# Optimization experiments

Measured on AMD Instinct MI355X. Metric: run time of the kernel, lower is better.

Reference implementation:

```python
import jax, jax.numpy as jnp
import numpy as np

N, E, R, D, S = 50000, 400000, 500, 128, 20
P = R * S
EPS = 1e-5

def setup_inputs() -> dict:
    key = jax.random.key(0)
    ks = jax.random.split(key, 20)
    xav = (2.0 / (D + D)) ** 0.5  # xavier_normal std for square layers
    def W(k):
        return jax.random.normal(k, (D, D), jnp.float32) * xav
    inp = {
        'ent_emb': jax.random.normal(ks[0], (N, D), jnp.float32),
        'rel_emb': jax.random.normal(ks[1], (R, D), jnp.float32),
        'edge_Wo': W(ks[2]), 'edge_bo': jnp.zeros((D,), jnp.float32),
        'edge_Wi': W(ks[3]), 'edge_bi': jnp.zeros((D,), jnp.float32),
        'edge_g': jnp.ones((D,), jnp.float32), 'edge_b': jnp.zeros((D,), jnp.float32),
        'node_Wo': W(ks[4]), 'node_bo': jnp.zeros((D,), jnp.float32),
        'node_Wi': W(ks[5]), 'node_bi': jnp.zeros((D,), jnp.float32),
        'node_g': jnp.ones((D,), jnp.float32), 'node_b': jnp.zeros((D,), jnp.float32),
        'comp_Wo': W(ks[6]), 'comp_bo': jnp.zeros((D,), jnp.float32),
        'comp_Wi': W(ks[7]), 'comp_bi': jnp.zeros((D,), jnp.float32),
        'comp_g': jnp.ones((D,), jnp.float32), 'comp_b': jnp.zeros((D,), jnp.float32),
        'relW': W(ks[8]), 'relb': jnp.zeros((D,), jnp.float32),
        'src': jax.random.randint(ks[9], (E,), 0, N),
        'dst': jax.random.randint(ks[10], (E,), 0, N),
        'etype': jax.random.randint(ks[11], (E,), 0, R),
        'heads': jax.random.randint(ks[13], (P,), 0, N),
        'tails': jax.random.randint(ks[14], (P,), 0, N),
        'rel_ids': jnp.repeat(jnp.arange(R), S),  # S sampled pairs per relation
    }
    in_mask = jax.random.randint(ks[12], (E,), 0, 2).astype(bool)
    inp['in_mask'] = in_mask
    inp['out_mask'] = ~in_mask  # DGL forward/reverse edge split: complementary masks
    return inp

def _edge_softmax(logit, dst, n):
    # segment softmax over edges grouped by destination node
    m = jax.ops.segment_max(logit, dst, num_segments=n)
    e = jnp.exp(logit - m[dst])
    s = jax.ops.segment_sum(e, dst, num_segments=n)
    return e / s[dst]

def _in_out(x, in_m, out_m, Wo, bo, Wi, bi):
    ho = x @ Wo.T + bo
    hi = x @ Wi.T + bi
    h = jnp.where(out_m[:, None], ho, jnp.zeros((), x.dtype))
    return jnp.where(in_m[:, None], hi, h)  # in-edges overwrite (masks disjoint)

def _bn_tanh(x, g, b):
    # training-mode BatchNorm1d (biased batch variance) + Tanh
    mu = jnp.mean(x, 0)
    var = jnp.mean(jnp.square(x - mu), 0)
    return jnp.tanh(g * (x - mu) * jax.lax.rsqrt(var + EPS) + b)

def reference(ent_emb, rel_emb,
              edge_Wo, edge_bo, edge_Wi, edge_bi, edge_g, edge_b,
              node_Wo, node_bo, node_Wi, node_bi, node_g, node_b,
              comp_Wo, comp_bo, comp_Wi, comp_bi, comp_g, comp_b,
              relW, relb,
              src, dst, etype, in_mask, out_mask, heads, tails, rel_ids):
    n = ent_emb.shape[0]
    r = rel_emb.shape[0]
    rel_e = rel_emb[etype]      # [E,D]
    e_src = ent_emb[src]        # [E,D]
    e_dst = ent_emb[dst]        # [E,D]

    # EdgeLayer: attn = e_dot_v(rel_e, dst_emb)
    a = _edge_softmax(jnp.sum(rel_e * e_dst, -1), dst, n)
    h = _in_out(rel_e, in_mask, out_mask, edge_Wo, edge_bo, edge_Wi, edge_bi) * a[:, None]
    edge_ent = _bn_tanh(jax.ops.segment_sum(h, dst, num_segments=n), edge_g, edge_b)

    # NodeLayer: attn = u_dot_v, message = src emb
    a = _edge_softmax(jnp.sum(e_src * e_dst, -1), dst, n)
    h = _in_out(e_src, in_mask, out_mask, node_Wo, node_bo, node_Wi, node_bi) * a[:, None]
    node_ent = _bn_tanh(jax.ops.segment_sum(h, dst, num_segments=n), node_g, node_b)

    # CompLayer (comp_fn='mul'): comp = u_mul_e, attn = e_dot_v(comp, dst)
    comp = e_src * rel_e
    a = _edge_softmax(jnp.sum(comp * e_dst, -1), dst, n)
    h = _in_out(comp, in_mask, out_mask, comp_Wo, comp_bo, comp_Wi, comp_bi) * a[:, None]
    comp_ent = _bn_tanh(jax.ops.segment_sum(h, dst, num_segments=n), comp_g, comp_b)

    final_ent = comp_ent + ent_emb + edge_ent + node_ent

    # update_relations: mean of w_rel_edge(tail - head) per relation
    pair = ent_emb[tails] - ent_emb[heads]          # [P,D]
    upd = pair @ relW.T + relb
    ssum = jax.ops.segment_sum(upd, rel_ids, num_segments=r)
    cnt = jax.ops.segment_sum(jnp.ones((rel_ids.shape[0],), jnp.float32), rel_ids, num_segments=r)
    cnt = jnp.maximum(cnt, 1.0)[:, None]
    final_rel = rel_emb + jnp.tanh(ssum / cnt)
    return final_ent, final_rel
```

## Files before the change

kernel.cpp:

```cpp
#include <hip/hip_runtime.h>
#include <stdint.h>

#define DN 128
#define NSTAT 64

typedef short s16x8 __attribute__((ext_vector_type(8)));
typedef float f32x4 __attribute__((ext_vector_type(4)));

__device__ __forceinline__ float bfs(unsigned short u){ return __uint_as_float(((uint32_t)u) << 16); }
__device__ __forceinline__ uint32_t f2bf(float f){
    uint32_t x = __float_as_uint(f);
    return (x + 0x7FFFu + ((x >> 16) & 1u)) >> 16;
}
__device__ __forceinline__ uint32_t packbf(float a, float b){ return f2bf(a) | (f2bf(b) << 16); }
__device__ __forceinline__ float tanh_(float x){
    float e = __expf(2.0f * x);
    return 1.0f - 2.0f / (e + 1.0f);
}

struct WC { const float* src[6]; };
__global__ void k_pre(const int* dst, int* counts,
                      const uint32_t* maskw, int nwords, int* flag,
                      WC wc, unsigned short* wcv, int E){
    int gid = blockIdx.x * 256 + threadIdx.x;
    if (gid < E) atomicAdd(&counts[dst[gid]], 1);
    if (gid < nwords && maskw[gid] > 1u) atomicOr(flag, 1);
    if (gid < 6 * 16384){
        int m = gid >> 14, o = gid & 16383;
        wcv[(size_t)m * 16384 + o] = (unsigned short)f2bf(wc.src[m][o]);
    }
}

__global__ void k_scan_a(const int* counts, int* bsums){
    int t = threadIdx.x;
    int s = counts[blockIdx.x * 256 + t];
    #pragma unroll
    for (int o = 32; o; o >>= 1) s += __shfl_xor(s, o);
    __shared__ int wsum[4];
    if ((t & 63) == 0) wsum[t >> 6] = s;
    __syncthreads();
    if (t == 0) bsums[blockIdx.x] = wsum[0] + wsum[1] + wsum[2] + wsum[3];
}

__global__ void k_scan_bc(const int* counts, const int* bsums, int nsb,
                          int* rowst, int* cursor, int npad, int E){
    __shared__ int pref;
    __shared__ int wsum[4];
    __shared__ int buf[256];
    int t = threadIdx.x, bid = blockIdx.x;
    int s = (t < bid && t < nsb) ? bsums[t] : 0;
    #pragma unroll
    for (int o = 32; o; o >>= 1) s += __shfl_xor(s, o);
    if ((t & 63) == 0) wsum[t >> 6] = s;
    __syncthreads();
    if (t == 0) pref = wsum[0] + wsum[1] + wsum[2] + wsum[3];
    int i = bid * 256 + t;
    int c = counts[i];
    buf[t] = c;
    __syncthreads();
    for (int o = 1; o < 256; o <<= 1){
        int add = (t >= o) ? buf[t - o] : 0;
        __syncthreads();
        buf[t] += add;
        __syncthreads();
    }
    int rsv = buf[t] - c + pref;
    rowst[i] = rsv; cursor[i] = rsv;
    if (i == npad - 1) rowst[npad] = E;
}

__global__ void k_scatter(const int* dst, const int* src, const int* etype,
                          const unsigned char* mask8, const int* flagp,
                          int* cursor, uint32_t* epack, int E){
    int e = blockIdx.x * blockDim.x + threadIdx.x;
    if (e >= E) return;
    int bmode = *flagp;
    int mk = bmode ? (int)mask8[e] : ((const int*)mask8)[e];
    int pos = atomicAdd(&cursor[dst[e]], 1);
    epack[pos] = ((uint32_t)src[e] << 16) | ((uint32_t)etype[e] << 1) | (uint32_t)(mk != 0);
}

__global__ __launch_bounds__(256)
void k_node(const float4* ent4, const float4* rel4,
            const uint32_t* epack, const int* rowst,
            uint32_t* Sw, float* Rv, int Nn, int npad)
{
    int t = threadIdx.x, lane = t & 63, wv = t >> 6;
    int v = blockIdx.x * 4 + wv;
    if (v >= npad) return;
    int sl = lane & 31, half = lane >> 5;

    float4 d4 = {0.f, 0.f, 0.f, 0.f};
    int deg = 0, rs = 0;
    if (v < Nn){
        rs = rowst[v]; deg = rowst[v + 1] - rs;
        d4 = ent4[(size_t)v * 32 + sl];
    }
    float m0 = -1e30f, m1 = -1e30f, m2 = -1e30f;
    float si0 = 0, si1 = 0, si2 = 0, so0 = 0, so1 = 0, so2 = 0;
    float4 aI0 = {0,0,0,0}, aO0 = {0,0,0,0};
    float4 aI1 = {0,0,0,0}, aO1 = {0,0,0,0};
    float4 aI2 = {0,0,0,0}, aO2 = {0,0,0,0};

    for (int base = 0; base < deg; base += 64){
        int nb = min(64, deg - base);
        uint32_t pk = 0;
        if (lane < nb) pk = epack[rs + base + lane];
        int npair = (nb + 1) >> 1;
        for (int j = 0; j < npair; ++j){
            int ei = 2 * j + half;
            uint32_t w = (uint32_t)__shfl((int)pk, ei);
            int sj = (int)(w >> 16);
            int tj = (int)((w >> 1) & 0x7FFF);
            float mk = (float)(w & 1u);
            bool pad = (ei >= nb);
            float4 s4 = ent4[(size_t)sj * 32 + sl];
            float4 r4 = rel4[(size_t)tj * 32 + sl];
            float4 c4 = { s4.x*r4.x, s4.y*r4.y, s4.z*r4.z, s4.w*r4.w };
            float p0 = r4.x*d4.x + r4.y*d4.y + r4.z*d4.z + r4.w*d4.w;
            float p1 = s4.x*d4.x + s4.y*d4.y + s4.z*d4.z + s4.w*d4.w;
            float p2 = c4.x*d4.x + c4.y*d4.y + c4.z*d4.z + c4.w*d4.w;
            #pragma unroll
            for (int o = 1; o < 32; o <<= 1){
                p0 += __shfl_xor(p0, o);
                p1 += __shfl_xor(p1, o);
                p2 += __shfl_xor(p2, o);
            }
            if (pad){ p0 = -1e38f; p1 = -1e38f; p2 = -1e38f; }
            {
                float nm = fmaxf(m0, p0);
                float f = __expf(m0 - nm);
                si0 *= f; so0 *= f;
                aI0.x*=f; aI0.y*=f; aI0.z*=f; aI0.w*=f;
                aO0.x*=f; aO0.y*=f; aO0.z*=f; aO0.w*=f;
                m0 = nm;
                float e = __expf(p0 - m0);
                float ein = e * mk, eout = e - ein;
                si0 += ein; so0 += eout;
                aI0.x += ein*r4.x; aI0.y += ein*r4.y; aI0.z += ein*r4.z; aI0.w += ein*r4.w;
                aO0.x += eout*r4.x; aO0.y += eout*r4.y; aO0.z += eout*r4.z; aO0.w += eout*r4.w;
            }
            {
                float nm = fmaxf(m1, p1);
                float f = __expf(m1 - nm);
                si1 *= f; so1 *= f;
                aI1.x*=f; aI1.y*=f; aI1.z*=f; aI1.w*=f;
                aO1.x*=f; aO1.y*=f; aO1.z*=f; aO1.w*=f;
                m1 = nm;
                float e = __expf(p1 - m1);
                float ein = e * mk, eout = e - ein;
                si1 += ein; so1 += eout;
                aI1.x += ein*s4.x; aI1.y += ein*s4.y; aI1.z += ein*s4.z; aI1.w += ein*s4.w;
                aO1.x += eout*s4.x; aO1.y += eout*s4.y; aO1.z += eout*s4.z; aO1.w += eout*s4.w;
            }
            {
                float nm = fmaxf(m2, p2);
                float f = __expf(m2 - nm);
                si2 *= f; so2 *= f;
                aI2.x*=f; aI2.y*=f; aI2.z*=f; aI2.w*=f;
                aO2.x*=f; aO2.y*=f; aO2.z*=f; aO2.w*=f;
                m2 = nm;
                float e = __expf(p2 - m2);
                float ein = e * mk, eout = e - ein;
                si2 += ein; so2 += eout;
                aI2.x += ein*c4.x; aI2.y += ein*c4.y; aI2.z += ein*c4.z; aI2.w += ein*c4.w;
                aO2.x += eout*c4.x; aO2.y += eout*c4.y; aO2.z += eout*c4.z; aO2.w += eout*c4.w;
            }
        }
    }

    {
        float mo, nm, f;
#define MRG(m, si, so, aI, aO)                                            \
        mo = __shfl_xor(m, 32);                                           \
        nm = fmaxf(m, mo);                                                \
        f = __expf(m - nm);                                               \
        si *= f; so *= f;                                                 \
        aI.x*=f; aI.y*=f; aI.z*=f; aI.w*=f;                               \
        aO.x*=f; aO.y*=f; aO.z*=f; aO.w*=f;                               \
        si += __shfl_xor(si, 32);                                         \
        so += __shfl_xor(so, 32);                                         \
        aI.x += __shfl_xor(aI.x, 32); aI.y += __shfl_xor(aI.y, 32);       \
        aI.z += __shfl_xor(aI.z, 32); aI.w += __shfl_xor(aI.w, 32);       \
        aO.x += __shfl_xor(aO.x, 32); aO.y += __shfl_xor(aO.y, 32);       \
        aO.z += __shfl_xor(aO.z, 32); aO.w += __shfl_xor(aO.w, 32);
        MRG(m0, si0, so0, aI0, aO0)
        MRG(m1, si1, so1, aI1, aO1)
        MRG(m2, si2, so2, aI2, aO2)
#undef MRG
    }

    if (half == 0){
        uint2* S2 = (uint2*)Sw;
        size_t s2 = (size_t)npad * 32;
        size_t wi = (size_t)v * 32 + sl;
        float st, inv;
        st = si0 + so0; inv = st > 0.f ? 1.f / st : 0.f;
        S2[0*s2 + wi] = make_uint2(packbf(aI0.x*inv, aI0.y*inv), packbf(aI0.z*inv, aI0.w*inv));
        S2[1*s2 + wi] = make_uint2(packbf(aO0.x*inv, aO0.y*inv), packbf(aO0.z*inv, aO0.w*inv));
        float ri0 = si0*inv, ro0 = so0*inv;
        st = si1 + so1; inv = st > 0.f ? 1.f / st : 0.f;
        S2[2*s2 + wi] = make_uint2(packbf(aI1.x*inv, aI1.y*inv), packbf(aI1.z*inv, aI1.w*inv));
        S2[3*s2 + wi] = make_uint2(packbf(aO1.x*inv, aO1.y*inv), packbf(aO1.z*inv, aO1.w*inv));
        float ri1 = si1*inv, ro1 = so1*inv;
        st = si2 + so2; inv = st > 0.f ? 1.f / st : 0.f;
        S2[4*s2 + wi] = make_uint2(packbf(aI2.x*inv, aI2.y*inv), packbf(aI2.z*inv, aI2.w*inv));
        S2[5*s2 + wi] = make_uint2(packbf(aO2.x*inv, aO2.y*inv), packbf(aO2.z*inv, aO2.w*inv));
        float ri2 = si2*inv, ro2 = so2*inv;
        if (sl == 0){
            Rv[0*(size_t)npad + v] = ri0; Rv[1*(size_t)npad + v] = ro0;
            Rv[2*(size_t)npad + v] = ri1; Rv[3*(size_t)npad + v] = ro1;
            Rv[4*(size_t)npad + v] = ri2; Rv[5*(size_t)npad + v] = ro2;
        }
    }
}

struct GArgs {
    const short* Wi[3]; const short* Wo[3];
    const float* bi[3]; const float* bo[3];
};

__global__ __launch_bounds__(256)
void k_gemm(GArgs ga, const short* Sb, const float* Rv, unsigned short* P,
            float* statsP, int npad, int Nn)
{
    __shared__ float lsum[128], lsq[128];
    int t = threadIdx.x;
    if (t < 128){ lsum[t] = 0.f; lsq[t] = 0.f; }
    __syncthreads();
    int l = blockIdx.y;
    int lane = t & 63, wv = t >> 6;
    int lo = lane & 15, hi = lane >> 4;
    int r0 = blockIdx.x * 64 + wv * 16;
    size_t sstride = (size_t)npad * DN;
    const short* Sin  = Sb + (size_t)(2*l)   * sstride;
    const short* Sout = Sb + (size_t)(2*l+1) * sstride;
    const short* Wi = ga.Wi[l]; const short* Wo = ga.Wo[l];

    s16x8 ain[4], aout[4];
    #pragma unroll
    for (int kb = 0; kb < 4; ++kb){
        size_t o = (size_t)(r0 + lo) * DN + kb*32 + hi*8;
        ain[kb]  = *(const s16x8*)(Sin + o);
        aout[kb] = *(const s16x8*)(Sout + o);
    }
    float rin[4], rout[4];
    const float* RvI = Rv + (size_t)(2*l)   * npad;
    const float* RvO = Rv + (size_t)(2*l+1) * npad;
    #pragma unroll
    for (int rg = 0; rg < 4; ++rg){
        int vr = r0 + hi*4 + rg;
        rin[rg] = RvI[vr]; rout[rg] = RvO[vr];
    }
    unsigned short* Pl = P + (size_t)l * sstride;

    #pragma unroll
    for (int ct = 0; ct < 8; ++ct){
        f32x4 acc = {0.f, 0.f, 0.f, 0.f};
        #pragma unroll
        for (int kb = 0; kb < 4; ++kb){
            size_t wo = (size_t)(ct*16 + lo) * DN + kb*32 + hi*8;
            s16x8 bwi = *(const s16x8*)(Wi + wo);
            acc = __builtin_amdgcn_mfma_f32_16x16x32_bf16(ain[kb], bwi, acc, 0, 0, 0);
            s16x8 bwo = *(const s16x8*)(Wo + wo);
            acc = __builtin_amdgcn_mfma_f32_16x16x32_bf16(aout[kb], bwo, acc, 0, 0, 0);
        }
        int j = ct*16 + lo;
        float biv = ga.bi[l][j], bov = ga.bo[l][j];
        float cs = 0.f, cq = 0.f;
        #pragma unroll
        for (int rg = 0; rg < 4; ++rg){
            float pv = acc[rg] + rin[rg]*biv + rout[rg]*bov;
            Pl[(size_t)(r0 + hi*4 + rg) * DN + j] = (unsigned short)f2bf(pv);
            cs += pv; cq += pv*pv;
        }
        cs += __shfl_xor(cs, 16); cs += __shfl_xor(cs, 32);
        cq += __shfl_xor(cq, 16); cq += __shfl_xor(cq, 32);
        if (lane < 16){ atomicAdd(&lsum[j], cs); atomicAdd(&lsq[j], cq); }
    }
    __syncthreads();
    float* stats = statsP + (size_t)((blockIdx.x ^ (blockIdx.y << 4)) & (NSTAT-1)) * 768;
    if (t < 128){
        atomicAdd(&stats[l*128 + t], lsum[t]);
        atomicAdd(&stats[384 + l*128 + t], lsq[t]);
    }
}

struct BArgs { const float* g[3]; const float* b[3]; };

__global__ void k_bn(BArgs ba, const float* statsP, float* bnAB, int Nn){
    int t = threadIdx.x;
    if (t >= 384) return;
    float su = 0.f, sq = 0.f;
    for (int k = 0; k < NSTAT; ++k){
        su += statsP[(size_t)k * 768 + t];
        sq += statsP[(size_t)k * 768 + 384 + t];
    }
    int l = t >> 7;
    float mu = su / (float)Nn;
    float var = fmaxf(sq / (float)Nn - mu*mu, 0.f);
    float inv = rsqrtf(var + 1e-5f);
    float g = ba.g[l][t & 127], b = ba.b[l][t & 127];
    bnAB[t] = g * inv;
    bnAB[384 + t] = b - mu * g * inv;
}

__global__ __launch_bounds__(256)
void k_fin(const unsigned short* Pb, const float* bnAB,
           const float* ent, const float* relW, const float* relb,
           const float* rel, const int* heads, const int* tails,
           float* outp, int Nn, int npad, int FB, int Sp)
{
    int t = threadIdx.x, bid = blockIdx.x;
    if (bid < FB){
        __shared__ float sAB[768];
        for (int i = t; i < 768; i += 256) sAB[i] = bnAB[i];
        __syncthreads();
        int gid = bid * 256 + t;
        if (gid >= Nn * 32) return;
        int v = gid >> 5, q4 = (gid & 31) * 4;
        size_t pst = (size_t)npad * DN;
        size_t pb = (size_t)v * DN + q4;
        ushort4 p0 = *(const ushort4*)(Pb + pb);
        ushort4 p1 = *(const ushort4*)(Pb + pst + pb);
        ushort4 p2 = *(const ushort4*)(Pb + 2*pst + pb);
        float4 e4 = *(const float4*)(ent + (size_t)v * DN + q4);
        float pe[4] = { e4.x, e4.y, e4.z, e4.w };
        unsigned short pu[3][4] = { {p0.x, p0.y, p0.z, p0.w},
                                    {p1.x, p1.y, p1.z, p1.w},
                                    {p2.x, p2.y, p2.z, p2.w} };
        float o[4];
        #pragma unroll
        for (int q = 0; q < 4; ++q){
            float s = pe[q];
            #pragma unroll
            for (int l = 0; l < 3; ++l){
                int jj = l*128 + q4 + q;
                s += tanh_(sAB[jj] * bfs(pu[l][q]) + sAB[384 + jj]);
            }
            o[q] = s;
        }
        float4 ov = { o[0], o[1], o[2], o[3] };
        *(float4*)(outp + (size_t)v * DN + q4) = ov;
    } else {
        __shared__ float mp[256];
        int rr = (bid - FB) * 2 + (t >> 7);
        int j = t & 127;
        float acc = 0.f;
        for (int s = 0; s < Sp; ++s){
            int p = rr * Sp + s;
            acc += ent[(size_t)tails[p] * DN + j] - ent[(size_t)heads[p] * DN + j];
        }
        mp[t] = acc / (float)Sp;
        __syncthreads();
        float dot = relb[j];
        const float4* wr = (const float4*)(relW + (size_t)j * DN);
        const float* mpr = mp + (t >> 7) * 128;
        #pragma unroll 8
        for (int kb = 0; kb < 32; ++kb){
            float4 w = wr[kb];
            dot += mpr[kb*4+0]*w.x + mpr[kb*4+1]*w.y + mpr[kb*4+2]*w.z + mpr[kb*4+3]*w.w;
        }
        outp[(size_t)Nn * DN + (size_t)rr * DN + j] = rel[(size_t)rr * DN + j] + tanh_(dot);
    }
}

extern "C" void kernel_launch(void* const* d_in, const int* in_sizes, int n_in,
                              void* d_out, int out_size, void* d_ws, size_t ws_size,
                              hipStream_t stream)
{
    const float* entf = (const float*)d_in[0];
    const float* relf = (const float*)d_in[1];
    const float* eWo = (const float*)d_in[2];  const float* ebo = (const float*)d_in[3];
    const float* eWi = (const float*)d_in[4];  const float* ebi = (const float*)d_in[5];
    const float* eg  = (const float*)d_in[6];  const float* eb  = (const float*)d_in[7];
    const float* nWo = (const float*)d_in[8];  const float* nbo = (const float*)d_in[9];
    const float* nWi = (const float*)d_in[10]; const float* nbi = (const float*)d_in[11];
    const float* ng  = (const float*)d_in[12]; const float* nb_ = (const float*)d_in[13];
    const float* cWo = (const float*)d_in[14]; const float* cbo = (const float*)d_in[15];
    const float* cWi = (const float*)d_in[16]; const float* cbi = (const float*)d_in[17];
    const float* cg  = (const float*)d_in[18]; const float* cb  = (const float*)d_in[19];
    const float* relWs  = (const float*)d_in[20];
    const float* relb32 = (const float*)d_in[21];
    const int* srcp   = (const int*)d_in[22];
    const int* dstp   = (const int*)d_in[23];
    const int* etyp   = (const int*)d_in[24];
    const int* headsp = (const int*)d_in[25];
    const int* tailsp = (const int*)d_in[26];
    const unsigned char* mask8 = (const unsigned char*)d_in[28];

    int Nn = in_sizes[0] / DN;
    int Rr = in_sizes[1] / DN;
    int E  = in_sizes[22];
    int Pp = in_sizes[25];
    int Sp = Pp / Rr;
    int npad = ((Nn + 255) / 256) * 256;
    int nsb = npad / 256;

    char* w = (char*)d_ws; size_t off = 0;
    auto carve = [&](size_t b) -> void* {
        void* p = w + off; off = (off + b + 255) & ~(size_t)255; return p;
    };
    int*   flag   = (int*)  carve(4);
    int*   counts = (int*)  carve((size_t)npad * 4);
    float* statsP = (float*)carve((size_t)NSTAT * 768 * 4);
    size_t zlen = off;
    int*   rowst  = (int*)  carve((size_t)(npad + 1) * 4);
    int*   cursor = (int*)  carve((size_t)npad * 4);
    uint32_t* epack = (uint32_t*)carve((size_t)E * 4);
    int*   bsums  = (int*)  carve(1024 * 4);
    unsigned short* wcv = (unsigned short*)carve((size_t)6 * 16384 * 2);
    short* Sb     = (short*)carve((size_t)6 * npad * DN * 2);
    unsigned short* Pb = (unsigned short*)carve((size_t)3 * npad * DN * 2);
    float* Rv     = (float*)carve((size_t)6 * npad * 4);
    float* bnAB   = (float*)carve(768 * 4);

    hipMemsetAsync(d_ws, 0, zlen, stream);

    WC wc; wc.src[0] = eWi; wc.src[1] = nWi; wc.src[2] = cWi;
           wc.src[3] = eWo; wc.src[4] = nWo; wc.src[5] = cWo;
    int nwords = 4096;
    k_pre<<<(E + 255) / 256, 256, 0, stream>>>(dstp, counts, (const uint32_t*)mask8,
                                               nwords, flag, wc, wcv, E);
    k_scan_a<<<nsb, 256, 0, stream>>>(counts, bsums);
    k_scan_bc<<<nsb, 256, 0, stream>>>(counts, bsums, nsb, rowst, cursor, npad, E);
    k_scatter<<<(E + 255) / 256, 256, 0, stream>>>(dstp, srcp, etyp, mask8, flag,
                                                   cursor, epack, E);

    k_node<<<npad / 4, 256, 0, stream>>>((const float4*)entf, (const float4*)relf,
                                         epack, rowst, (uint32_t*)Sb, Rv, Nn, npad);

    GArgs ga;
    ga.Wi[0] = (const short*)(wcv + 0*16384);
    ga.Wi[1] = (const short*)(wcv + 1*16384);
    ga.Wi[2] = (const short*)(wcv + 2*16384);
    ga.Wo[0] = (const short*)(wcv + 3*16384);
    ga.Wo[1] = (const short*)(wcv + 4*16384);
    ga.Wo[2] = (const short*)(wcv + 5*16384);
    ga.bi[0] = ebi; ga.bi[1] = nbi; ga.bi[2] = cbi;
    ga.bo[0] = ebo; ga.bo[1] = nbo; ga.bo[2] = cbo;
    k_gemm<<<dim3(npad / 64, 3), 256, 0, stream>>>(ga, Sb, Rv, Pb, statsP, npad, Nn);

    BArgs ba;
    ba.g[0] = eg; ba.g[1] = ng; ba.g[2] = cg;
    ba.b[0] = eb; ba.b[1] = nb_; ba.b[2] = cb;
    k_bn<<<1, 384, 0, stream>>>(ba, statsP, bnAB, Nn);

    int FB = (Nn * 32 + 255) / 256;
    int grid = FB + Rr / 2;
    k_fin<<<grid, 256, 0, stream>>>(Pb, bnAB, entf, relWs, relb32, relf,
                                    headsp, tailsp, (float*)d_out, Nn, npad, FB, Sp);
}
```

Measured before the change: 391.9 us.

## Process four edges per wave in node kernel and widen GEMM row tiles

The node aggregation kernel now handles four edges at once per wavefront, using 16 lanes per edge with 8-float vectors, and merges partial results across lane groups at the end. The online-softmax rescale is skipped unless a new logit exceeds the running max by more than 20, which drops most exp and multiply work per edge. The GEMM kernel now computes four 16-row tiles per wave and reuses the loaded weight fragments across them, with launch bounds set for one block. The cost is more registers and fewer GEMM blocks, and rows could be dropped if npad is not a multiple of 256.

```diff
diff --git a/kernel.cpp b/kernel.cpp
--- a/kernel.cpp
+++ b/kernel.cpp
@@ -6,6 +6,7 @@
 
 typedef short s16x8 __attribute__((ext_vector_type(8)));
 typedef float f32x4 __attribute__((ext_vector_type(4)));
+typedef float f32x8 __attribute__((ext_vector_type(8)));
 
 __device__ __forceinline__ float bfs(unsigned short u){ return __uint_as_float(((uint32_t)u) << 16); }
 __device__ __forceinline__ uint32_t f2bf(float f){
@@ -81,132 +82,148 @@
 }
 
 __global__ __launch_bounds__(256)
-void k_node(const float4* ent4, const float4* rel4,
+void k_node(const f32x8* ent8, const f32x8* rel8,
             const uint32_t* epack, const int* rowst,
             uint32_t* Sw, float* Rv, int Nn, int npad)
 {
     int t = threadIdx.x, lane = t & 63, wv = t >> 6;
     int v = blockIdx.x * 4 + wv;
     if (v >= npad) return;
-    int sl = lane & 31, half = lane >> 5;
-
-    float4 d4 = {0.f, 0.f, 0.f, 0.f};
+    int sl = lane & 15, grp = lane >> 4;
+
+    f32x8 d8 = {0,0,0,0,0,0,0,0};
     int deg = 0, rs = 0;
     if (v < Nn){
         rs = rowst[v]; deg = rowst[v + 1] - rs;
-        d4 = ent4[(size_t)v * 32 + sl];
+        d8 = ent8[(size_t)v * 16 + sl];
     }
     float m0 = -1e30f, m1 = -1e30f, m2 = -1e30f;
     float si0 = 0, si1 = 0, si2 = 0, so0 = 0, so1 = 0, so2 = 0;
-    float4 aI0 = {0,0,0,0}, aO0 = {0,0,0,0};
-    float4 aI1 = {0,0,0,0}, aO1 = {0,0,0,0};
-    float4 aI2 = {0,0,0,0}, aO2 = {0,0,0,0};
+    f32x8 aI0 = {0,0,0,0,0,0,0,0}, aO0 = {0,0,0,0,0,0,0,0};
+    f32x8 aI1 = {0,0,0,0,0,0,0,0}, aO1 = {0,0,0,0,0,0,0,0};
+    f32x8 aI2 = {0,0,0,0,0,0,0,0}, aO2 = {0,0,0,0,0,0,0,0};
 
     for (int base = 0; base < deg; base += 64){
         int nb = min(64, deg - base);
         uint32_t pk = 0;
         if (lane < nb) pk = epack[rs + base + lane];
-        int npair = (nb + 1) >> 1;
-        for (int j = 0; j < npair; ++j){
-            int ei = 2 * j + half;
+        int ngrp = (nb + 3) >> 2;
+        for (int j = 0; j < ngrp; ++j){
+            int ei = 4 * j + grp;
             uint32_t w = (uint32_t)__shfl((int)pk, ei);
             int sj = (int)(w >> 16);
             int tj = (int)((w >> 1) & 0x7FFF);
             float mk = (float)(w & 1u);
-            bool pad = (ei >= nb);
-            float4 s4 = ent4[(size_t)sj * 32 + sl];
-            float4 r4 = rel4[(size_t)tj * 32 + sl];
-            float4 c4 = { s4.x*r4.x, s4.y*r4.y, s4.z*r4.z, s4.w*r4.w };
-            float p0 = r4.x*d4.x + r4.y*d4.y + r4.z*d4.z + r4.w*d4.w;
-            float p1 = s4.x*d4.x + s4.y*d4.y + s4.z*d4.z + s4.w*d4.w;
-            float p2 = c4.x*d4.x + c4.y*d4.y + c4.z*d4.z + c4.w*d4.w;
-            #pragma unroll
-            for (int o = 1; o < 32; o <<= 1){
+            f32x8 s8 = ent8[(size_t)sj * 16 + sl];
+            f32x8 r8 = rel8[(size_t)tj * 16 + sl];
+            f32x8 c8;
+            #pragma unroll
+            for (int q = 0; q < 8; ++q) c8[q] = s8[q] * r8[q];
+            float p0 = 0.f, p1 = 0.f, p2 = 0.f;
+            #pragma unroll
+            for (int q = 0; q < 8; ++q){
+                p0 += r8[q] * d8[q];
+                p1 += s8[q] * d8[q];
+                p2 += c8[q] * d8[q];
+            }
+            #pragma unroll
+            for (int o = 1; o < 16; o <<= 1){
                 p0 += __shfl_xor(p0, o);
                 p1 += __shfl_xor(p1, o);
                 p2 += __shfl_xor(p2, o);
             }
-            if (pad){ p0 = -1e38f; p1 = -1e38f; p2 = -1e38f; }
+            if (ei >= nb){ p0 = -1e38f; p1 = -1e38f; p2 = -1e38f; }
             {
-                float nm = fmaxf(m0, p0);
-                float f = __expf(m0 - nm);
-                si0 *= f; so0 *= f;
-                aI0.x*=f; aI0.y*=f; aI0.z*=f; aI0.w*=f;
-                aO0.x*=f; aO0.y*=f; aO0.z*=f; aO0.w*=f;
-                m0 = nm;
+                if (__any(p0 > m0 + 20.f)){
+                    float nm = fmaxf(m0, p0);
+                    float f = __expf(m0 - nm);
+                    si0 *= f; so0 *= f;
+                    #pragma unroll
+                    for (int q = 0; q < 8; ++q){ aI0[q] *= f; aO0[q] *= f; }
+                    m0 = nm;
+                }
                 float e = __expf(p0 - m0);
                 float ein = e * mk, eout = e - ein;
                 si0 += ein; so0 += eout;
-                aI0.x += ein*r4.x; aI0.y += ein*r4.y; aI0.z += ein*r4.z; aI0.w += ein*r4.w;
-                aO0.x += eout*r4.x; aO0.y += eout*r4.y; aO0.z += eout*r4.z; aO0.w += eout*r4.w;
+                #pragma unroll
+                for (int q = 0; q < 8; ++q){ aI0[q] += ein * r8[q]; aO0[q] += eout * r8[q]; }
             }
             {
-                float nm = fmaxf(m1, p1);
-                float f = __expf(m1 - nm);
-                si1 *= f; so1 *= f;
-                aI1.x*=f; aI1.y*=f; aI1.z*=f; aI1.w*=f;
-                aO1.x*=f; aO1.y*=f; aO1.z*=f; aO1.w*=f;
-                m1 = nm;
+                if (__any(p1 > m1 + 20.f)){
+                    float nm = fmaxf(m1, p1);
+                    float f = __expf(m1 - nm);
+                    si1 *= f; so1 *= f;
+                    #pragma unroll
+                    for (int q = 0; q < 8; ++q){ aI1[q] *= f; aO1[q] *= f; }
+                    m1 = nm;
+                }
                 float e = __expf(p1 - m1);
                 float ein = e * mk, eout = e - ein;
                 si1 += ein; so1 += eout;
-                aI1.x += ein*s4.x; aI1.y += ein*s4.y; aI1.z += ein*s4.z; aI1.w += ein*s4.w;
-                aO1.x += eout*s4.x; aO1.y += eout*s4.y; aO1.z += eout*s4.z; aO1.w += eout*s4.w;
+                #pragma unroll
+                for (int q = 0; q < 8; ++q){ aI1[q] += ein * s8[q]; aO1[q] += eout * s8[q]; }
             }
             {
-                float nm = fmaxf(m2, p2);
-                float f = __expf(m2 - nm);
-                si2 *= f; so2 *= f;
-                aI2.x*=f; aI2.y*=f; aI2.z*=f; aI2.w*=f;
-                aO2.x*=f; aO2.y*=f; aO2.z*=f; aO2.w*=f;
-                m2 = nm;
+                if (__any(p2 > m2 + 20.f)){
+                    float nm = fmaxf(m2, p2);
+                    float f = __expf(m2 - nm);
+                    si2 *= f; so2 *= f;
+                    #pragma unroll
+                    for (int q = 0; q < 8; ++q){ aI2[q] *= f; aO2[q] *= f; }
+                    m2 = nm;
+                }
                 float e = __expf(p2 - m2);
                 float ein = e * mk, eout = e - ein;
                 si2 += ein; so2 += eout;
-                aI2.x += ein*c4.x; aI2.y += ein*c4.y; aI2.z += ein*c4.z; aI2.w += ein*c4.w;
-                aO2.x += eout*c4.x; aO2.y += eout*c4.y; aO2.z += eout*c4.z; aO2.w += eout*c4.w;
-            }
-        }
-    }
-
-    {
-        float mo, nm, f;
-#define MRG(m, si, so, aI, aO)                                            \
-        mo = __shfl_xor(m, 32);                                           \
-        nm = fmaxf(m, mo);                                                \
-        f = __expf(m - nm);                                               \
-        si *= f; so *= f;                                                 \
-        aI.x*=f; aI.y*=f; aI.z*=f; aI.w*=f;                               \
-        aO.x*=f; aO.y*=f; aO.z*=f; aO.w*=f;                               \
-        si += __shfl_xor(si, 32);                                         \
-        so += __shfl_xor(so, 32);                                         \
-        aI.x += __shfl_xor(aI.x, 32); aI.y += __shfl_xor(aI.y, 32);       \
-        aI.z += __shfl_xor(aI.z, 32); aI.w += __shfl_xor(aI.w, 32);       \
-        aO.x += __shfl_xor(aO.x, 32); aO.y += __shfl_xor(aO.y, 32);       \
-        aO.z += __shfl_xor(aO.z, 32); aO.w += __shfl_xor(aO.w, 32);
-        MRG(m0, si0, so0, aI0, aO0)
-        MRG(m1, si1, so1, aI1, aO1)
-        MRG(m2, si2, so2, aI2, aO2)
-#undef MRG
-    }
-
-    if (half == 0){
-        uint2* S2 = (uint2*)Sw;
-        size_t s2 = (size_t)npad * 32;
-        size_t wi = (size_t)v * 32 + sl;
+                #pragma unroll
+                for (int q = 0; q < 8; ++q){ aI2[q] += ein * c8[q]; aO2[q] += eout * c8[q]; }
+            }
+        }
+    }
+
+#define MRG8(OFF, m, si, so, aI, aO) {                                     \
+        float mo = __shfl_xor(m, OFF);                                     \
+        float nm = fmaxf(m, mo);                                           \
+        float f = __expf(m - nm);                                          \
+        si *= f; so *= f;                                                  \
+        _Pragma("unroll")                                                  \
+        for (int q = 0; q < 8; ++q){ aI[q] *= f; aO[q] *= f; }             \
+        si += __shfl_xor(si, OFF);                                         \
+        so += __shfl_xor(so, OFF);                                         \
+        _Pragma("unroll")                                                  \
+        for (int q = 0; q < 8; ++q){                                       \
+            aI[q] += __shfl_xor(aI[q], OFF);                               \
+            aO[q] += __shfl_xor(aO[q], OFF);                               \
+        }                                                                  \
+        m = nm; }
+    MRG8(16, m0, si0, so0, aI0, aO0)
+    MRG8(16, m1, si1, so1, aI1, aO1)
+    MRG8(16, m2, si2, so2, aI2, aO2)
+    MRG8(32, m0, si0, so0, aI0, aO0)
+    MRG8(32, m1, si1, so1, aI1, aO1)
+    MRG8(32, m2, si2, so2, aI2, aO2)
+#undef MRG8
+
+    if (lane < 16){
+        uint4* S4 = (uint4*)Sw;
+        size_t s4 = (size_t)npad * 16;
+        size_t wi = (size_t)v * 16 + sl;
         float st, inv;
+#define PK8(A, I) make_uint4(packbf(A[0]*I, A[1]*I), packbf(A[2]*I, A[3]*I), \
+                             packbf(A[4]*I, A[5]*I), packbf(A[6]*I, A[7]*I))
         st = si0 + so0; inv = st > 0.f ? 1.f / st : 0.f;
-        S2[0*s2 + wi] = make_uint2(packbf(aI0.x*inv, aI0.y*inv), packbf(aI0.z*inv, aI0.w*inv));
-        S2[1*s2 + wi] = make_uint2(packbf(aO0.x*inv, aO0.y*inv), packbf(aO0.z*inv, aO0.w*inv));
+        S4[0*s4 + wi] = PK8(aI0, inv);
+        S4[1*s4 + wi] = PK8(aO0, inv);
         float ri0 = si0*inv, ro0 = so0*inv;
         st = si1 + so1; inv = st > 0.f ? 1.f / st : 0.f;
-        S2[2*s2 + wi] = make_uint2(packbf(aI1.x*inv, aI1.y*inv), packbf(aI1.z*inv, aI1.w*inv));
-        S2[3*s2 + wi] = make_uint2(packbf(aO1.x*inv, aO1.y*inv), packbf(aO1.z*inv, aO1.w*inv));
+        S4[2*s4 + wi] = PK8(aI1, inv);
+        S4[3*s4 + wi] = PK8(aO1, inv);
         float ri1 = si1*inv, ro1 = so1*inv;
         st = si2 + so2; inv = st > 0.f ? 1.f / st : 0.f;
-        S2[4*s2 + wi] = make_uint2(packbf(aI2.x*inv, aI2.y*inv), packbf(aI2.z*inv, aI2.w*inv));
-        S2[5*s2 + wi] = make_uint2(packbf(aO2.x*inv, aO2.y*inv), packbf(aO2.z*inv, aO2.w*inv));
+        S4[4*s4 + wi] = PK8(aI2, inv);
+        S4[5*s4 + wi] = PK8(aO2, inv);
         float ri2 = si2*inv, ro2 = so2*inv;
+#undef PK8
         if (sl == 0){
             Rv[0*(size_t)npad + v] = ri0; Rv[1*(size_t)npad + v] = ro0;
             Rv[2*(size_t)npad + v] = ri1; Rv[3*(size_t)npad + v] = ro1;
@@ -220,7 +237,7 @@
     const float* bi[3]; const float* bo[3];
 };
 
-__global__ __launch_bounds__(256)
+__global__ __launch_bounds__(256, 1)
 void k_gemm(GArgs ga, const short* Sb, const float* Rv, unsigned short* P,
             float* statsP, int npad, int Nn)
 {
@@ -231,48 +248,59 @@
     int l = blockIdx.y;
     int lane = t & 63, wv = t >> 6;
     int lo = lane & 15, hi = lane >> 4;
-    int r0 = blockIdx.x * 64 + wv * 16;
+    int wr0 = blockIdx.x * 256 + wv * 64;
     size_t sstride = (size_t)npad * DN;
     const short* Sin  = Sb + (size_t)(2*l)   * sstride;
     const short* Sout = Sb + (size_t)(2*l+1) * sstride;
     const short* Wi = ga.Wi[l]; const short* Wo = ga.Wo[l];
 
-    s16x8 ain[4], aout[4];
+    s16x8 ain[4][4], aout[4][4];
     #pragma unroll
-    for (int kb = 0; kb < 4; ++kb){
-        size_t o = (size_t)(r0 + lo) * DN + kb*32 + hi*8;
-        ain[kb]  = *(const s16x8*)(Sin + o);
-        aout[kb] = *(const s16x8*)(Sout + o);
-    }
-    float rin[4], rout[4];
+    for (int rt = 0; rt < 4; ++rt)
+        #pragma unroll
+        for (int kb = 0; kb < 4; ++kb){
+            size_t o = (size_t)(wr0 + rt*16 + lo) * DN + kb*32 + hi*8;
+            ain[rt][kb]  = *(const s16x8*)(Sin + o);
+            aout[rt][kb] = *(const s16x8*)(Sout + o);
+        }
+    float rin[4][4], rout[4][4];
     const float* RvI = Rv + (size_t)(2*l)   * npad;
     const float* RvO = Rv + (size_t)(2*l+1) * npad;
     #pragma unroll
-    for (int rg = 0; rg < 4; ++rg){
-        int vr = r0 + hi*4 + rg;
-        rin[rg] = RvI[vr]; rout[rg] = RvO[vr];
-    }
+    for (int rt = 0; rt < 4; ++rt)
+        #pragma unroll
+        for (int rg = 0; rg < 4; ++rg){
+            int vr = wr0 + rt*16 + hi*4 + rg;
+            rin[rt][rg] = RvI[vr]; rout[rt][rg] = RvO[vr];
+        }
     unsigned short* Pl = P + (size_t)l * sstride;
 
     #pragma unroll
     for (int ct = 0; ct < 8; ++ct){
-        f32x4 acc = {0.f, 0.f, 0.f, 0.f};
+        s16x8 bwi[4], bwo[4];
         #pragma unroll
         for (int kb = 0; kb < 4; ++kb){
-            size_t wo = (size_t)(ct*16 + lo) * DN + kb*32 + hi*8;
-            s16x8 bwi = *(const s16x8*)(Wi + wo);
-            acc = __builtin_amdgcn_mfma_f32_16x16x32_bf16(ain[kb], bwi, acc, 0, 0, 0);
-            s16x8 bwo = *(const s16x8*)(Wo + wo);
-            acc = __builtin_amdgcn_mfma_f32_16x16x32_bf16(aout[kb], bwo, acc, 0, 0, 0);
+            size_t wo_ = (size_t)(ct*16 + lo) * DN + kb*32 + hi*8;
+            bwi[kb] = *(const s16x8*)(Wi + wo_);
+            bwo[kb] = *(const s16x8*)(Wo + wo_);
         }
         int j = ct*16 + lo;
         float biv = ga.bi[l][j], bov = ga.bo[l][j];
         float cs = 0.f, cq = 0.f;
         #pragma unroll
-        for (int rg = 0; rg < 4; ++rg){
-            float pv = acc[rg] + rin[rg]*biv + rout[rg]*bov;
-            Pl[(size_t)(r0 + hi*4 + rg) * DN + j] = (unsigned short)f2bf(pv);
-            cs += pv; cq += pv*pv;
+        for (int rt = 0; rt < 4; ++rt){
+            f32x4 acc = {0.f, 0.f, 0.f, 0.f};
+            #pragma unroll
+            for (int kb = 0; kb < 4; ++kb){
+                acc = __builtin_amdgcn_mfma_f32_16x16x32_bf16(ain[rt][kb], bwi[kb], acc, 0, 0, 0);
+                acc = __builtin_amdgcn_mfma_f32_16x16x32_bf16(aout[rt][kb], bwo[kb], acc, 0, 0, 0);
+            }
+            #pragma unroll
+            for (int rg = 0; rg < 4; ++rg){
+                float pv = acc[rg] + rin[rt][rg]*biv + rout[rt][rg]*bov;
+                Pl[(size_t)(wr0 + rt*16 + hi*4 + rg) * DN + j] = (unsigned short)f2bf(pv);
+                cs += pv; cq += pv*pv;
+            }
         }
         cs += __shfl_xor(cs, 16); cs += __shfl_xor(cs, 32);
         cq += __shfl_xor(cq, 16); cq += __shfl_xor(cq, 32);
@@ -427,7 +455,7 @@
     k_scatter<<<(E + 255) / 256, 256, 0, stream>>>(dstp, srcp, etyp, mask8, flag,
                                                    cursor, epack, E);
 
-    k_node<<<npad / 4, 256, 0, stream>>>((const float4*)entf, (const float4*)relf,
+    k_node<<<npad / 4, 256, 0, stream>>>((const f32x8*)entf, (const f32x8*)relf,
                                          epack, rowst, (uint32_t*)Sb, Rv, Nn, npad);
 
     GArgs ga;
@@ -439,7 +467,7 @@
     ga.Wo[2] = (const short*)(wcv + 5*16384);
     ga.bi[0] = ebi; ga.bi[1] = nbi; ga.bi[2] = cbi;
     ga.bo[0] = ebo; ga.bo[1] = nbo; ga.bo[2] = cbo;
-    k_gemm<<<dim3(npad / 64, 3), 256, 0, stream>>>(ga, Sb, Rv, Pb, statsP, npad, Nn);
+    k_gemm<<<dim3(npad / 256, 3), 256, 0, stream>>>(ga, Sb, Rv, Pb, statsP, npad, Nn);
 
     BArgs ba;
     ba.g[0] = eg; ba.g[1] = ng; ba.g[2] = cg;
```

New measurement: 361.7 us. 1.08x faster.

## Prefetch next edge gathers, lazily rescale softmax, and enlarge GEMM row tiles

Applied to the files above, without the earlier changes.

In the node aggregation kernel, the gathers for the next edge pair are issued before the current pair is processed, which hides memory latency. The online-softmax rescale now runs only when some lane's logit exceeds the running max by more than 20, which skips most exp and multiply work. The GEMM kernel gives each wave 64 rows instead of 16 and reuses the weight fragments across four row tiles, so weight loads are cut fourfold, but register pressure rises and the grid has fewer blocks. The lazy rescale keeps a stale max, so the correctness of the exponent bound relies on logits staying moderate, and npad must be divisible by 256.

```diff
diff --git a/kernel.cpp b/kernel.cpp
--- a/kernel.cpp
+++ b/kernel.cpp
@@ -107,15 +107,21 @@
         uint32_t pk = 0;
         if (lane < nb) pk = epack[rs + base + lane];
         int npair = (nb + 1) >> 1;
+        uint32_t w = (uint32_t)__shfl((int)pk, half);
+        float4 s4 = ent4[(size_t)(w >> 16) * 32 + sl];
+        float4 r4 = rel4[(size_t)((w >> 1) & 0x7FFF) * 32 + sl];
+        float mk = (float)(w & 1u);
+        bool pad = (half >= nb);
         for (int j = 0; j < npair; ++j){
-            int ei = 2 * j + half;
-            uint32_t w = (uint32_t)__shfl((int)pk, ei);
-            int sj = (int)(w >> 16);
-            int tj = (int)((w >> 1) & 0x7FFF);
-            float mk = (float)(w & 1u);
-            bool pad = (ei >= nb);
-            float4 s4 = ent4[(size_t)sj * 32 + sl];
-            float4 r4 = rel4[(size_t)tj * 32 + sl];
+            float4 s4n = s4, r4n = r4; float mkn = 0.f; bool padn = true;
+            if (j + 1 < npair){
+                int ein = 2 * (j + 1) + half;
+                uint32_t wn = (uint32_t)__shfl((int)pk, ein);
+                s4n = ent4[(size_t)(wn >> 16) * 32 + sl];
+                r4n = rel4[(size_t)((wn >> 1) & 0x7FFF) * 32 + sl];
+                mkn = (float)(wn & 1u);
+                padn = (ein >= nb);
+            }
             float4 c4 = { s4.x*r4.x, s4.y*r4.y, s4.z*r4.z, s4.w*r4.w };
             float p0 = r4.x*d4.x + r4.y*d4.y + r4.z*d4.z + r4.w*d4.w;
             float p1 = s4.x*d4.x + s4.y*d4.y + s4.z*d4.z + s4.w*d4.w;
@@ -128,44 +134,51 @@
             }
             if (pad){ p0 = -1e38f; p1 = -1e38f; p2 = -1e38f; }
             {
-                float nm = fmaxf(m0, p0);
-                float f = __expf(m0 - nm);
-                si0 *= f; so0 *= f;
-                aI0.x*=f; aI0.y*=f; aI0.z*=f; aI0.w*=f;
-                aO0.x*=f; aO0.y*=f; aO0.z*=f; aO0.w*=f;
-                m0 = nm;
+                if (__any(p0 > m0 + 20.f)){
+                    float nm = fmaxf(m0, p0);
+                    float f = __expf(m0 - nm);
+                    si0 *= f; so0 *= f;
+                    aI0.x*=f; aI0.y*=f; aI0.z*=f; aI0.w*=f;
+                    aO0.x*=f; aO0.y*=f; aO0.z*=f; aO0.w*=f;
+                    m0 = nm;
+                }
                 float e = __expf(p0 - m0);
-                float ein = e * mk, eout = e - ein;
-                si0 += ein; so0 += eout;
-                aI0.x += ein*r4.x; aI0.y += ein*r4.y; aI0.z += ein*r4.z; aI0.w += ein*r4.w;
+                float ein_ = e * mk, eout = e - ein_;
+                si0 += ein_; so0 += eout;
+                aI0.x += ein_*r4.x; aI0.y += ein_*r4.y; aI0.z += ein_*r4.z; aI0.w += ein_*r4.w;
                 aO0.x += eout*r4.x; aO0.y += eout*r4.y; aO0.z += eout*r4.z; aO0.w += eout*r4.w;
             }
             {
-                float nm = fmaxf(m1, p1);
-                float f = __expf(m1 - nm);
-                si1 *= f; so1 *= f;
-                aI1.x*=f; aI1.y*=f; aI1.z*=f; aI1.w*=f;
-                aO1.x*=f; aO1.y*=f; aO1.z*=f; aO1.w*=f;
-                m1 = nm;
+                if (__any(p1 > m1 + 20.f)){
+                    float nm = fmaxf(m1, p1);
+                    float f = __expf(m1 - nm);
+                    si1 *= f; so1 *= f;
+                    aI1.x*=f; aI1.y*=f; aI1.z*=f; aI1.w*=f;
+                    aO1.x*=f; aO1.y*=f; aO1.z*=f; aO1.w*=f;
+                    m1 = nm;
+                }
                 float e = __expf(p1 - m1);
-                float ein = e * mk, eout = e - ein;
-                si1 += ein; so1 += eout;
-                aI1.x += ein*s4.x; aI1.y += ein*s4.y; aI1.z += ein*s4.z; aI1.w += ein*s4.w;
+                float ein_ = e * mk, eout = e - ein_;
+                si1 += ein_; so1 += eout;
+                aI1.x += ein_*s4.x; aI1.y += ein_*s4.y; aI1.z += ein_*s4.z; aI1.w += ein_*s4.w;
                 aO1.x += eout*s4.x; aO1.y += eout*s4.y; aO1.z += eout*s4.z; aO1.w += eout*s4.w;
             }
             {
-                float nm = fmaxf(m2, p2);
-                float f = __expf(m2 - nm);
-                si2 *= f; so2 *= f;
-                aI2.x*=f; aI2.y*=f; aI2.z*=f; aI2.w*=f;
-                aO2.x*=f; aO2.y*=f; aO2.z*=f; aO2.w*=f;
-                m2 = nm;
+                if (__any(p2 > m2 + 20.f)){
+                    float nm = fmaxf(m2, p2);
+                    float f = __expf(m2 - nm);
+                    si2 *= f; so2 *= f;
+                    aI2.x*=f; aI2.y*=f; aI2.z*=f; aI2.w*=f;
+                    aO2.x*=f; aO2.y*=f; aO2.z*=f; aO2.w*=f;
+                    m2 = nm;
+                }
                 float e = __expf(p2 - m2);
-                float ein = e * mk, eout = e - ein;
-                si2 += ein; so2 += eout;
-                aI2.x += ein*c4.x; aI2.y += ein*c4.y; aI2.z += ein*c4.z; aI2.w += ein*c4.w;
+                float ein_ = e * mk, eout = e - ein_;
+                si2 += ein_; so2 += eout;
+                aI2.x += ein_*c4.x; aI2.y += ein_*c4.y; aI2.z += ein_*c4.z; aI2.w += ein_*c4.w;
                 aO2.x += eout*c4.x; aO2.y += eout*c4.y; aO2.z += eout*c4.z; aO2.w += eout*c4.w;
             }
+            s4 = s4n; r4 = r4n; mk = mkn; pad = padn;
         }
     }
 
@@ -220,7 +233,7 @@
     const float* bi[3]; const float* bo[3];
 };
 
-__global__ __launch_bounds__(256)
+__global__ __launch_bounds__(256, 1)
 void k_gemm(GArgs ga, const short* Sb, const float* Rv, unsigned short* P,
             float* statsP, int npad, int Nn)
 {
@@ -231,48 +244,59 @@
     int l = blockIdx.y;
     int lane = t & 63, wv = t >> 6;
     int lo = lane & 15, hi = lane >> 4;
-    int r0 = blockIdx.x * 64 + wv * 16;
+    int wr0 = blockIdx.x * 256 + wv * 64;
     size_t sstride = (size_t)npad * DN;
     const short* Sin  = Sb + (size_t)(2*l)   * sstride;
     const short* Sout = Sb + (size_t)(2*l+1) * sstride;
     const short* Wi = ga.Wi[l]; const short* Wo = ga.Wo[l];
 
-    s16x8 ain[4], aout[4];
+    s16x8 ain[4][4], aout[4][4];
     #pragma unroll
-    for (int kb = 0; kb < 4; ++kb){
-        size_t o = (size_t)(r0 + lo) * DN + kb*32 + hi*8;
-        ain[kb]  = *(const s16x8*)(Sin + o);
-        aout[kb] = *(const s16x8*)(Sout + o);
-    }
-    float rin[4], rout[4];
+    for (int rt = 0; rt < 4; ++rt)
+        #pragma unroll
+        for (int kb = 0; kb < 4; ++kb){
+            size_t o = (size_t)(wr0 + rt*16 + lo) * DN + kb*32 + hi*8;
+            ain[rt][kb]  = *(const s16x8*)(Sin + o);
+            aout[rt][kb] = *(const s16x8*)(Sout + o);
+        }
+    float rin[4][4], rout[4][4];
     const float* RvI = Rv + (size_t)(2*l)   * npad;
     const float* RvO = Rv + (size_t)(2*l+1) * npad;
     #pragma unroll
-    for (int rg = 0; rg < 4; ++rg){
-        int vr = r0 + hi*4 + rg;
-        rin[rg] = RvI[vr]; rout[rg] = RvO[vr];
-    }
+    for (int rt = 0; rt < 4; ++rt)
+        #pragma unroll
+        for (int rg = 0; rg < 4; ++rg){
+            int vr = wr0 + rt*16 + hi*4 + rg;
+            rin[rt][rg] = RvI[vr]; rout[rt][rg] = RvO[vr];
+        }
     unsigned short* Pl = P + (size_t)l * sstride;
 
     #pragma unroll
     for (int ct = 0; ct < 8; ++ct){
-        f32x4 acc = {0.f, 0.f, 0.f, 0.f};
+        s16x8 bwi[4], bwo[4];
         #pragma unroll
         for (int kb = 0; kb < 4; ++kb){
-            size_t wo = (size_t)(ct*16 + lo) * DN + kb*32 + hi*8;
-            s16x8 bwi = *(const s16x8*)(Wi + wo);
-            acc = __builtin_amdgcn_mfma_f32_16x16x32_bf16(ain[kb], bwi, acc, 0, 0, 0);
-            s16x8 bwo = *(const s16x8*)(Wo + wo);
-            acc = __builtin_amdgcn_mfma_f32_16x16x32_bf16(aout[kb], bwo, acc, 0, 0, 0);
+            size_t wo_ = (size_t)(ct*16 + lo) * DN + kb*32 + hi*8;
+            bwi[kb] = *(const s16x8*)(Wi + wo_);
+            bwo[kb] = *(const s16x8*)(Wo + wo_);
         }
         int j = ct*16 + lo;
         float biv = ga.bi[l][j], bov = ga.bo[l][j];
         float cs = 0.f, cq = 0.f;
         #pragma unroll
-        for (int rg = 0; rg < 4; ++rg){
-            float pv = acc[rg] + rin[rg]*biv + rout[rg]*bov;
-            Pl[(size_t)(r0 + hi*4 + rg) * DN + j] = (unsigned short)f2bf(pv);
-            cs += pv; cq += pv*pv;
+        for (int rt = 0; rt < 4; ++rt){
+            f32x4 acc = {0.f, 0.f, 0.f, 0.f};
+            #pragma unroll
+            for (int kb = 0; kb < 4; ++kb){
+                acc = __builtin_amdgcn_mfma_f32_16x16x32_bf16(ain[rt][kb], bwi[kb], acc, 0, 0, 0);
+                acc = __builtin_amdgcn_mfma_f32_16x16x32_bf16(aout[rt][kb], bwo[kb], acc, 0, 0, 0);
+            }
+            #pragma unroll
+            for (int rg = 0; rg < 4; ++rg){
+                float pv = acc[rg] + rin[rt][rg]*biv + rout[rt][rg]*bov;
+                Pl[(size_t)(wr0 + rt*16 + hi*4 + rg) * DN + j] = (unsigned short)f2bf(pv);
+                cs += pv; cq += pv*pv;
+            }
         }
         cs += __shfl_xor(cs, 16); cs += __shfl_xor(cs, 32);
         cq += __shfl_xor(cq, 16); cq += __shfl_xor(cq, 32);
@@ -439,7 +463,7 @@
     ga.Wo[2] = (const short*)(wcv + 5*16384);
     ga.bi[0] = ebi; ga.bi[1] = nbi; ga.bi[2] = cbi;
     ga.bo[0] = ebo; ga.bo[1] = nbo; ga.bo[2] = cbo;
-    k_gemm<<<dim3(npad / 64, 3), 256, 0, stream>>>(ga, Sb, Rv, Pb, statsP, npad, Nn);
+    k_gemm<<<dim3(npad / 256, 3), 256, 0, stream>>>(ga, Sb, Rv, Pb, statsP, npad, Nn);
 
     BArgs ba;
     ba.g[0] = eg; ba.g[1] = ng; ba.g[2] = cg;
```

New measurement: 336.3 us. -14.2%, faster.
